# Performance work log

Hardware: AMD Instinct MI355X
Metric: run time of the kernel (lower is better)

## Reference

```python
import jax, jax.numpy as jnp
import numpy as np

B, L, D, H = 4, 1024, 1024, 16
HD = D // H  # head_dim = 64
SCALE = HD ** -0.5


def setup_inputs() -> dict:
    key = jax.random.key(0)
    k1, k2, k3, k4 = jax.random.split(key, 4)
    x = jax.random.normal(k1, (B, L, D), dtype=jnp.float32)
    # torch nn.Linear(dim, 3*dim): y = x @ W.T + b; we store W already transposed to [D, 3D]
    Wqkv = jax.random.normal(k2, (D, 3 * D), dtype=jnp.float32) * (D ** -0.5)
    bqkv = jax.random.normal(k3, (3 * D,), dtype=jnp.float32) * 0.02
    # distance_embedding: nn.Embedding(2*length - 1, head_dim)
    dist_emb = jax.random.normal(k4, (2 * L - 1, HD), dtype=jnp.float32) * 0.02
    return {"x": x, "Wqkv": Wqkv, "bqkv": bqkv, "dist_emb": dist_emb}


def reference(x, Wqkv, bqkv, dist_emb):
    b, l, d = x.shape
    # QKV projection -> [3, B, H, L, HD]
    qkv = (x @ Wqkv + bqkv).reshape(b, l, 3, H, HD).transpose(2, 0, 3, 1, 4)
    q, k, v = qkv[0], qkv[1], qkv[2]
    # raw attention scores: [B, H, L, L]
    scores = jnp.einsum("bhld,bhmd->bhlm", q, k)
    # relative position bias (relative_key_query branch)
    pos = jnp.arange(l)
    distance = pos[:, None] - pos[None, :]          # [L, L] in [-(L-1), L-1]
    pe = dist_emb[distance + (L - 1)]               # [L, L, HD]
    rel_q = jnp.einsum("bhld,lrd->bhlr", q, pe)
    rel_k = jnp.einsum("bhrd,lrd->bhlr", k, pe)
    scores = (scores + rel_q + rel_k) * SCALE
    probs = jax.nn.softmax(scores, axis=-1)
    out = jnp.einsum("bhlm,bhmd->bhld", probs, v)   # [B, H, L, HD]
    return out.transpose(0, 2, 1, 3).reshape(b, l, d)
```

## Files before the change

### kernel.cpp

```cpp
#include <hip/hip_runtime.h>
#include <hip/hip_bf16.h>
#include <math.h>

#define Bq 4
#define Lq 1024
#define Dq 1024
#define Hq 16
#define HDq 64
#define BHq (Bq * Hq)
#define HEAD_ELEMS ((size_t)BHq * Lq * HDq)

typedef short bf16x8 __attribute__((ext_vector_type(8)));
typedef _Float16 f16x8 __attribute__((ext_vector_type(8)));
typedef float f32x4 __attribute__((ext_vector_type(4)));
#define MFMA16B(A, B, C) __builtin_amdgcn_mfma_f32_16x16x32_bf16(A, B, C, 0, 0, 0)
#define MFMA16F(A, B, C) __builtin_amdgcn_mfma_f32_16x16x32_f16(A, B, C, 0, 0, 0)

__device__ __forceinline__ unsigned short f2bf(float x) {
  unsigned u = __builtin_bit_cast(unsigned, x);
  unsigned r = u + 0x7FFFu + ((u >> 16) & 1u);
  return (unsigned short)(r >> 16);
}
__device__ __forceinline__ float bf2f(unsigned short s) {
  unsigned u = ((unsigned)s) << 16;
  return __builtin_bit_cast(float, u);
}
__device__ __forceinline__ unsigned short f2h(float x) {
  _Float16 h = (_Float16)x;
  return __builtin_bit_cast(unsigned short, h);
}

__global__ __launch_bounds__(256) void x_prep(const float* __restrict__ X,
                                              unsigned short* __restrict__ Xh) {
  size_t i = (size_t)blockIdx.x * 256 + threadIdx.x;
  float4 f = *(const float4*)(X + i * 4);
  uint2 pk;
  pk.x = (unsigned)f2h(f.x) | ((unsigned)f2h(f.y) << 16);
  pk.y = (unsigned)f2h(f.z) | ((unsigned)f2h(f.w) << 16);
  *(uint2*)(Xh + i * 4) = pk;
}

__global__ __launch_bounds__(256) void wt_prep(const float* __restrict__ W,
                                               unsigned short* __restrict__ Wt) {
  __shared__ unsigned short tile[64 * 72];
  const int k0 = blockIdx.x * 64;
  const int n0 = blockIdx.y * 64;
  const int tid = threadIdx.x;
#pragma unroll
  for (int it = 0; it < 4; it++) {
    int idx = tid + it * 256;
    int r = idx >> 4, c4 = (idx & 15) * 4;
    float4 f = *(const float4*)(W + (size_t)(k0 + r) * 3072 + n0 + c4);
    unsigned w0 = (unsigned)f2h(f.x) | ((unsigned)f2h(f.y) << 16);
    unsigned w1 = (unsigned)f2h(f.z) | ((unsigned)f2h(f.w) << 16);
    *(unsigned*)&tile[r * 72 + c4] = w0;
    *(unsigned*)&tile[r * 72 + c4 + 2] = w1;
  }
  __syncthreads();
#pragma unroll
  for (int it = 0; it < 4; it++) {
    int u = tid + it * 256;
    int n = u >> 4, k4 = (u & 15) * 4;
    unsigned short e0 = tile[(k4 + 0) * 72 + n];
    unsigned short e1 = tile[(k4 + 1) * 72 + n];
    unsigned short e2 = tile[(k4 + 2) * 72 + n];
    unsigned short e3 = tile[(k4 + 3) * 72 + n];
    uint2 pk;
    pk.x = (unsigned)e0 | ((unsigned)e1 << 16);
    pk.y = (unsigned)e2 | ((unsigned)e3 << 16);
    *(uint2*)(Wt + (size_t)(n0 + n) * 1024 + k0 + k4) = pk;
  }
}

__global__ __launch_bounds__(256) void emb_prep(const float* __restrict__ e,
                                                unsigned short* __restrict__ o) {
  int i = blockIdx.x * 256 + threadIdx.x;
  if (i < 2047 * 64) o[i] = f2bf(e[i]);
}

__global__ __launch_bounds__(256, 2) void qkv_mfma(
    const unsigned short* __restrict__ Xh, const unsigned short* __restrict__ Wt,
    const float* __restrict__ bias, unsigned short* __restrict__ qkvg) {
  __shared__ __align__(16) char smem[32768];
  unsigned short* Asm = (unsigned short*)smem;
  unsigned short* Bsm = (unsigned short*)(smem + 8192);
  unsigned short* Cs  = (unsigned short*)smem;

  const int tid = threadIdx.x;
  const int w = tid >> 6, lane = tid & 63;
  const int col = lane & 15, quad = lane >> 4;
  const int wm = (w >> 1) * 64, wn = (w & 1) * 64;
  const int bn = blockIdx.x * 128, bm = blockIdx.y * 128;

  const unsigned short* Ag = Xh + (size_t)bm * 1024;
  const unsigned short* Bg = Wt + (size_t)bn * 1024;
  const int ldrow = w * 32 + (lane >> 2);
  const int ldoff = (lane & 3) * 8;

  f32x4 acc[4][4];
#pragma unroll
  for (int i = 0; i < 4; i++)
#pragma unroll
    for (int j = 0; j < 4; j++) acc[i][j] = (f32x4){0.f, 0.f, 0.f, 0.f};

  for (int k0 = 0; k0 < 1024; k0 += 32) {
    __syncthreads();
#pragma unroll
    for (int it = 0; it < 2; it++) {
      const unsigned short* ga = Ag + (size_t)(ldrow + it * 16) * 1024 + k0 + ldoff;
      const unsigned short* gb = Bg + (size_t)(ldrow + it * 16) * 1024 + k0 + ldoff;
      __builtin_amdgcn_global_load_lds(
          (const __attribute__((address_space(1))) unsigned*)ga,
          (__attribute__((address_space(3))) unsigned*)(Asm + (w * 32 + it * 16) * 32),
          16, 0, 0);
      __builtin_amdgcn_global_load_lds(
          (const __attribute__((address_space(1))) unsigned*)gb,
          (__attribute__((address_space(3))) unsigned*)(Bsm + (w * 32 + it * 16) * 32),
          16, 0, 0);
    }
    __syncthreads();
    f16x8 af[4], bf[4];
#pragma unroll
    for (int i = 0; i < 4; i++)
      af[i] = *(const f16x8*)&Asm[(wm + i * 16 + col) * 32 + quad * 8];
#pragma unroll
    for (int j = 0; j < 4; j++)
      bf[j] = *(const f16x8*)&Bsm[(wn + j * 16 + col) * 32 + quad * 8];
#pragma unroll
    for (int i = 0; i < 4; i++)
#pragma unroll
      for (int j = 0; j < 4; j++)
        acc[i][j] = MFMA16F(af[i], bf[j], acc[i][j]);
  }

  float bj[4];
#pragma unroll
  for (int j = 0; j < 4; j++) bj[j] = bias[bn + wn + j * 16 + col];

  __syncthreads();
#pragma unroll
  for (int i = 0; i < 4; i++)
#pragma unroll
    for (int j = 0; j < 4; j++)
#pragma unroll
      for (int k = 0; k < 4; k++)
        Cs[(wm + i * 16 + quad * 4 + k) * 128 + wn + j * 16 + col] =
            f2bf(acc[i][j][k] + bj[j]);
  __syncthreads();

  const int t = bn >> 10;
  unsigned short* dst_base = qkvg + (size_t)t * HEAD_ELEMS;
#pragma unroll
  for (int it = 0; it < 8; it++) {
    int u = tid + it * 256;
    int row = u >> 4, c8 = (u & 15) * 8;
    int m = bm + row;
    int n = bn + c8;
    int b = m >> 10, l = m & 1023;
    int cc = n & 1023, h = cc >> 6, d0 = cc & 63;
    uint4 val = *(const uint4*)&Cs[row * 128 + c8];
    *(uint4*)(dst_base + (((size_t)(b * 16 + h) * 1024 + l) * 64 + d0)) = val;
  }
}

__global__ __launch_bounds__(256) void vt_prep_bf(const unsigned short* __restrict__ vg,
                                                  unsigned short* __restrict__ vtg) {
  __shared__ unsigned short tile[64 * 72];
  const int bh = blockIdx.x;
  const int rt = blockIdx.y * 64;
  const int tid = threadIdx.x;
  const unsigned short* src = vg + ((size_t)bh * Lq + rt) * HDq;
#pragma unroll
  for (int it = 0; it < 2; it++) {
    int idx = tid + it * 256;
    int r = idx >> 3, o = (idx & 7) * 8;
    *(uint4*)&tile[r * 72 + o] = *(const uint4*)(src + (size_t)r * 64 + o);
  }
  __syncthreads();
  unsigned short* dst = vtg + (size_t)bh * HDq * Lq;
#pragma unroll
  for (int it = 0; it < 4; it++) {
    int u = tid + it * 256;
    int d = u >> 4, r4 = (u & 15) * 4;
    unsigned short e0 = tile[(r4 + 0) * 72 + d];
    unsigned short e1 = tile[(r4 + 1) * 72 + d];
    unsigned short e2 = tile[(r4 + 2) * 72 + d];
    unsigned short e3 = tile[(r4 + 3) * 72 + d];
    uint2 pk;
    pk.x = (unsigned)e0 | ((unsigned)e1 << 16);
    pk.y = (unsigned)e2 | ((unsigned)e3 << 16);
    *(uint2*)(dst + (size_t)d * Lq + rt + r4) = pk;
  }
}

__global__ __launch_bounds__(256, 2) void attn_mfma(
    const unsigned short* __restrict__ qg, const unsigned short* __restrict__ kg,
    const unsigned short* __restrict__ vtg, const unsigned short* __restrict__ emb,
    float* __restrict__ out) {
  __shared__ __align__(16) char smem[54272];
  unsigned short* Qs  = (unsigned short*)smem;
  unsigned short* Ps  = (unsigned short*)smem;
  unsigned short* Ks  = (unsigned short*)(smem + 9216);
  unsigned short* VTs = (unsigned short*)(smem + 18432);
  unsigned short* Pb  = (unsigned short*)(smem + 27648);
  unsigned short* B12 = (unsigned short*)(smem + 36864);

  const int bh = blockIdx.x;
  const int l0 = blockIdx.y * 64;
  const int tid = threadIdx.x;
  const int w = tid >> 6, lane = tid & 63;
  const int col = lane & 15, quad = lane >> 4;
  const int lw = w * 16;

  const unsigned short* Qg = qg + ((size_t)bh * Lq + l0) * HDq;
  const unsigned short* Kg = kg + (size_t)bh * Lq * HDq;
  const unsigned short* VTgh = vtg + (size_t)bh * HDq * Lq;

#pragma unroll
  for (int it = 0; it < 2; it++) {
    int idx = tid + it * 256;
    int r = idx >> 3, o = (idx & 7) * 8;
    *(uint4*)&Qs[r * 72 + o] = *(const uint4*)(Qg + (size_t)r * 64 + o);
    int g = min(l0 + 1024 + r, 2046);
    *(uint4*)&Pb[r * 72 + o] = *(const uint4*)(emb + (size_t)g * 64 + o);
  }
  __syncthreads();

  bf16x8 qf[2];
#pragma unroll
  for (int ks = 0; ks < 2; ks++)
    qf[ks] = *(const bf16x8*)&Qs[(lw + col) * 72 + quad * 8 + ks * 32];

  bf16x8 sav[4][2];
#pragma unroll
  for (int dm = 0; dm < 4; dm++)
#pragma unroll
    for (int ks = 0; ks < 2; ks++)
      sav[dm][ks] = *(const bf16x8*)&Pb[(dm * 16 + col) * 72 + quad * 8 + ks * 32];

  f32x4 oacc[4];
#pragma unroll
  for (int nt = 0; nt < 4; nt++) oacc[nt] = (f32x4){0.f, 0.f, 0.f, 0.f};
  float mrow[4] = {-1e30f, -1e30f, -1e30f, -1e30f};
  float lrow[4] = {0.f, 0.f, 0.f, 0.f};

  for (int ch = 0; ch < 16; ch++) {
    const int r0 = ch * 64;
    __syncthreads();

#pragma unroll
    for (int it = 0; it < 2; it++) {
      int idx = tid + it * 256;
      int r = idx >> 3, o = (idx & 7) * 8;
      *(uint4*)&Ks[r * 72 + o] = *(const uint4*)(Kg + (size_t)(r0 + r) * 64 + o);
    }
#pragma unroll
    for (int it = 0; it < 2; it++) {
      int idx = tid + it * 256;
      int d = idx >> 3, o = (idx & 7) * 8;
      *(uint4*)&VTs[d * 72 + o] = *(const uint4*)(VTgh + (size_t)d * Lq + r0 + o);
    }
    const int pb0 = l0 - r0 + 960;
#pragma unroll
    for (int it = 0; it < 2; it++) {
      int idx = tid + it * 256;
      int r = idx >> 3, o = (idx & 7) * 8;
      *(uint4*)&Pb[r * 72 + o] = *(const uint4*)(emb + (size_t)(pb0 + r) * 64 + o);
    }
    __syncthreads();

    bf16x8 kf[4][2];
#pragma unroll
    for (int rt = 0; rt < 4; rt++)
#pragma unroll
      for (int ks = 0; ks < 2; ks++)
        kf[rt][ks] = *(const bf16x8*)&Ks[(rt * 16 + col) * 72 + quad * 8 + ks * 32];
    f32x4 sac[4];
#pragma unroll
    for (int rt = 0; rt < 4; rt++) {
      f32x4 z = (f32x4){0.f, 0.f, 0.f, 0.f};
      z = MFMA16B(qf[0], kf[rt][0], z);
      z = MFMA16B(qf[1], kf[rt][1], z);
      sac[rt] = z;
    }

    bf16x8 kaf[2];
#pragma unroll
    for (int ks = 0; ks < 2; ks++)
      kaf[ks] = *(const bf16x8*)&Ks[(lw + col) * 72 + quad * 8 + ks * 32];

    bf16x8 fresh[4][2];
#pragma unroll
    for (int dm = 0; dm < 4; dm++)
#pragma unroll
      for (int ks = 0; ks < 2; ks++)
        fresh[dm][ks] = *(const bf16x8*)&Pb[(dm * 16 + col) * 72 + quad * 8 + ks * 32];

#pragma unroll
    for (int dt = 0; dt < 8; dt++) {
      bf16x8 pbf0 = (dt < 4) ? fresh[dt & 3][0] : sav[dt & 3][0];
      bf16x8 pbf1 = (dt < 4) ? fresh[dt & 3][1] : sav[dt & 3][1];
      f32x4 z = (f32x4){0.f, 0.f, 0.f, 0.f};
      f32x4 y = (f32x4){0.f, 0.f, 0.f, 0.f};
      z = MFMA16B(qf[0], pbf0, z);
      z = MFMA16B(qf[1], pbf1, z);
      y = MFMA16B(kaf[0], pbf0, y);
      y = MFMA16B(kaf[1], pbf1, y);
      const int dcol = dt * 16 + col;
#pragma unroll
      for (int k = 0; k < 4; k++) {
        int l1 = lw + quad * 4 + k;
        int r1 = l1 - dcol + 63;
        if (r1 >= 0 && r1 < 64) B12[l1 * 136 + 2 * r1] = f2bf(z[k]);
        int r2 = lw + quad * 4 + k;
        int l2 = dcol - 63 + r2;
        if (l2 >= 0 && l2 < 64) B12[l2 * 136 + 2 * r2 + 1] = f2bf(y[k]);
      }
    }
#pragma unroll
    for (int dm = 0; dm < 4; dm++)
#pragma unroll
      for (int ks = 0; ks < 2; ks++)
        sav[dm][ks] = fresh[dm][ks];
    __syncthreads();

    float p[4][4];
    float alpha[4];
#pragma unroll
    for (int k = 0; k < 4; k++) {
      int l1 = lw + quad * 4 + k;
      float st[4];
#pragma unroll
      for (int rt = 0; rt < 4; rt++) {
        int r = rt * 16 + col;
        unsigned pr = *(const unsigned*)&B12[l1 * 136 + 2 * r];
        float bias = bf2f((unsigned short)(pr & 0xFFFFu)) +
                     bf2f((unsigned short)(pr >> 16));
        st[rt] = (sac[rt][k] + bias) * 0.125f;
      }
      float mx = fmaxf(fmaxf(st[0], st[1]), fmaxf(st[2], st[3]));
      mx = fmaxf(mx, __shfl_xor(mx, 1));
      mx = fmaxf(mx, __shfl_xor(mx, 2));
      mx = fmaxf(mx, __shfl_xor(mx, 4));
      mx = fmaxf(mx, __shfl_xor(mx, 8));
      float mnew = fmaxf(mrow[k], mx);
      float a = __expf(mrow[k] - mnew);
      mrow[k] = mnew;
      alpha[k] = a;
      float ls = 0.f;
#pragma unroll
      for (int rt = 0; rt < 4; rt++) {
        p[rt][k] = __expf(st[rt] - mnew);
        ls += p[rt][k];
      }
      lrow[k] = lrow[k] * a + ls;
    }
#pragma unroll
    for (int nt = 0; nt < 4; nt++)
#pragma unroll
      for (int k = 0; k < 4; k++) oacc[nt][k] *= alpha[k];

#pragma unroll
    for (int rt = 0; rt < 4; rt++)
#pragma unroll
      for (int k = 0; k < 4; k++)
        Ps[(lw + quad * 4 + k) * 72 + rt * 16 + col] = f2bf(p[rt][k]);

    bf16x8 pf[2];
#pragma unroll
    for (int ks = 0; ks < 2; ks++)
      pf[ks] = *(const bf16x8*)&Ps[(lw + col) * 72 + quad * 8 + ks * 32];
#pragma unroll
    for (int nt = 0; nt < 4; nt++) {
      bf16x8 v0 = *(const bf16x8*)&VTs[(nt * 16 + col) * 72 + quad * 8];
      bf16x8 v1 = *(const bf16x8*)&VTs[(nt * 16 + col) * 72 + quad * 8 + 32];
      oacc[nt] = MFMA16B(pf[0], v0, oacc[nt]);
      oacc[nt] = MFMA16B(pf[1], v1, oacc[nt]);
    }
  }

  float inv[4];
#pragma unroll
  for (int k = 0; k < 4; k++) {
    float t = lrow[k];
    t += __shfl_xor(t, 1);
    t += __shfl_xor(t, 2);
    t += __shfl_xor(t, 4);
    t += __shfl_xor(t, 8);
    inv[k] = 1.0f / t;
  }
  const int b = bh >> 4, h = bh & 15;
#pragma unroll
  for (int nt = 0; nt < 4; nt++) {
#pragma unroll
    for (int k = 0; k < 4; k++) {
      int lg = l0 + lw + quad * 4 + k;
      int d = nt * 16 + col;
      out[(((size_t)b * Lq + lg) * Hq + h) * HDq + d] = oacc[nt][k] * inv[k];
    }
  }
}

extern "C" void kernel_launch(void* const* d_in, const int* in_sizes, int n_in,
                              void* d_out, int out_size, void* d_ws, size_t ws_size,
                              hipStream_t stream) {
  const float* x        = (const float*)d_in[0];
  const float* Wqkv     = (const float*)d_in[1];
  const float* bqkv     = (const float*)d_in[2];
  const float* dist_emb = (const float*)d_in[3];
  float* out = (float*)d_out;

  unsigned short* Xh   = (unsigned short*)d_ws;
  unsigned short* Wt   = (unsigned short*)((char*)d_ws + (8u << 20));
  unsigned short* qkvg = (unsigned short*)((char*)d_ws + (16u << 20));
  unsigned short* vtg  = (unsigned short*)((char*)d_ws + (40u << 20));
  unsigned short* emb  = (unsigned short*)((char*)d_ws + (48u << 20));

  x_prep<<<dim3(4096), dim3(256), 0, stream>>>(x, Xh);
  wt_prep<<<dim3(16, 48), dim3(256), 0, stream>>>(Wqkv, Wt);
  emb_prep<<<dim3(512), dim3(256), 0, stream>>>(dist_emb, emb);

  qkv_mfma<<<dim3(24, 32), dim3(256), 0, stream>>>(Xh, Wt, bqkv, qkvg);

  vt_prep_bf<<<dim3(BHq, Lq / 64), dim3(256), 0, stream>>>(qkvg + 2 * HEAD_ELEMS, vtg);

  attn_mfma<<<dim3(BHq, Lq / 64), dim3(256), 0, stream>>>(
      qkvg, qkvg + HEAD_ELEMS, vtg, emb, out);
}
```

Baseline: 262.7 us.

## Load MFMA fragments directly from global memory, drop LDS staging, use exp2

Q, K, V^T and distance-embedding fragments are now read straight from global memory into registers instead of being staged through shared memory. This removes the per-chunk LDS copies and their barriers, shrinks LDS from about 53 KB to 26 KB, and raises launch bounds to three blocks per CU. The softmax also folds log2(e) into the scale and uses a native exp2. In exchange each lane issues more scattered global loads that depend on L2 hits, with less latency hiding from the removed staging, and register pressure under the new bound may cause spills.

```diff
diff --git a/kernel.cpp b/kernel.cpp
--- a/kernel.cpp
+++ b/kernel.cpp
@@ -15,6 +15,12 @@
 typedef float f32x4 __attribute__((ext_vector_type(4)));
 #define MFMA16B(A, B, C) __builtin_amdgcn_mfma_f32_16x16x32_bf16(A, B, C, 0, 0, 0)
 #define MFMA16F(A, B, C) __builtin_amdgcn_mfma_f32_16x16x32_f16(A, B, C, 0, 0, 0)
+
+#if __has_builtin(__builtin_amdgcn_exp2f)
+#define EXP2F(x) __builtin_amdgcn_exp2f(x)
+#else
+#define EXP2F(x) __expf((x) * 0.6931471805599453f)
+#endif
 
 __device__ __forceinline__ unsigned short f2bf(float x) {
   unsigned u = __builtin_bit_cast(unsigned, x);
@@ -193,17 +199,13 @@
   }
 }
 
-__global__ __launch_bounds__(256, 2) void attn_mfma(
+__global__ __launch_bounds__(256, 3) void attn_mfma(
     const unsigned short* __restrict__ qg, const unsigned short* __restrict__ kg,
     const unsigned short* __restrict__ vtg, const unsigned short* __restrict__ emb,
     float* __restrict__ out) {
-  __shared__ __align__(16) char smem[54272];
-  unsigned short* Qs  = (unsigned short*)smem;
+  __shared__ __align__(16) char smem[26624];
   unsigned short* Ps  = (unsigned short*)smem;
-  unsigned short* Ks  = (unsigned short*)(smem + 9216);
-  unsigned short* VTs = (unsigned short*)(smem + 18432);
-  unsigned short* Pb  = (unsigned short*)(smem + 27648);
-  unsigned short* B12 = (unsigned short*)(smem + 36864);
+  unsigned short* B12 = (unsigned short*)(smem + 9216);
 
   const int bh = blockIdx.x;
   const int l0 = blockIdx.y * 64;
@@ -211,32 +213,26 @@
   const int w = tid >> 6, lane = tid & 63;
   const int col = lane & 15, quad = lane >> 4;
   const int lw = w * 16;
+  const int fo = quad * 8;
 
   const unsigned short* Qg = qg + ((size_t)bh * Lq + l0) * HDq;
-  const unsigned short* Kg = kg + (size_t)bh * Lq * HDq;
-  const unsigned short* VTgh = vtg + (size_t)bh * HDq * Lq;
-
-#pragma unroll
-  for (int it = 0; it < 2; it++) {
-    int idx = tid + it * 256;
-    int r = idx >> 3, o = (idx & 7) * 8;
-    *(uint4*)&Qs[r * 72 + o] = *(const uint4*)(Qg + (size_t)r * 64 + o);
-    int g = min(l0 + 1024 + r, 2046);
-    *(uint4*)&Pb[r * 72 + o] = *(const uint4*)(emb + (size_t)g * 64 + o);
-  }
-  __syncthreads();
+  const unsigned short* Kp = kg + (size_t)bh * Lq * HDq;
+  const unsigned short* Vp = vtg + (size_t)bh * HDq * Lq;
 
   bf16x8 qf[2];
 #pragma unroll
   for (int ks = 0; ks < 2; ks++)
-    qf[ks] = *(const bf16x8*)&Qs[(lw + col) * 72 + quad * 8 + ks * 32];
+    qf[ks] = *(const bf16x8*)(Qg + (size_t)(lw + col) * 64 + fo + ks * 32);
 
   bf16x8 sav[4][2];
 #pragma unroll
-  for (int dm = 0; dm < 4; dm++)
+  for (int dm = 0; dm < 4; dm++) {
+    int g = l0 + 1024 + dm * 16 + col;
+    g = (g > 2046) ? 2046 : g;
 #pragma unroll
     for (int ks = 0; ks < 2; ks++)
-      sav[dm][ks] = *(const bf16x8*)&Pb[(dm * 16 + col) * 72 + quad * 8 + ks * 32];
+      sav[dm][ks] = *(const bf16x8*)(emb + (size_t)g * 64 + fo + ks * 32);
+  }
 
   f32x4 oacc[4];
 #pragma unroll
@@ -244,37 +240,27 @@
   float mrow[4] = {-1e30f, -1e30f, -1e30f, -1e30f};
   float lrow[4] = {0.f, 0.f, 0.f, 0.f};
 
+  int pb0 = l0 + 960;
+
   for (int ch = 0; ch < 16; ch++) {
-    const int r0 = ch * 64;
-    __syncthreads();
-
-#pragma unroll
-    for (int it = 0; it < 2; it++) {
-      int idx = tid + it * 256;
-      int r = idx >> 3, o = (idx & 7) * 8;
-      *(uint4*)&Ks[r * 72 + o] = *(const uint4*)(Kg + (size_t)(r0 + r) * 64 + o);
-    }
-#pragma unroll
-    for (int it = 0; it < 2; it++) {
-      int idx = tid + it * 256;
-      int d = idx >> 3, o = (idx & 7) * 8;
-      *(uint4*)&VTs[d * 72 + o] = *(const uint4*)(VTgh + (size_t)d * Lq + r0 + o);
-    }
-    const int pb0 = l0 - r0 + 960;
-#pragma unroll
-    for (int it = 0; it < 2; it++) {
-      int idx = tid + it * 256;
-      int r = idx >> 3, o = (idx & 7) * 8;
-      *(uint4*)&Pb[r * 72 + o] = *(const uint4*)(emb + (size_t)(pb0 + r) * 64 + o);
-    }
-    __syncthreads();
-
     bf16x8 kf[4][2];
 #pragma unroll
     for (int rt = 0; rt < 4; rt++)
 #pragma unroll
       for (int ks = 0; ks < 2; ks++)
-        kf[rt][ks] = *(const bf16x8*)&Ks[(rt * 16 + col) * 72 + quad * 8 + ks * 32];
+        kf[rt][ks] = *(const bf16x8*)(Kp + (size_t)(rt * 16 + col) * 64 + fo + ks * 32);
+    bf16x8 kaf[2];
+#pragma unroll
+    for (int ks = 0; ks < 2; ks++)
+      kaf[ks] = *(const bf16x8*)(Kp + (size_t)(lw + col) * 64 + fo + ks * 32);
+    bf16x8 fresh[4][2];
+#pragma unroll
+    for (int dm = 0; dm < 4; dm++)
+#pragma unroll
+      for (int ks = 0; ks < 2; ks++)
+        fresh[dm][ks] =
+            *(const bf16x8*)(emb + (size_t)(pb0 + dm * 16 + col) * 64 + fo + ks * 32);
+
     f32x4 sac[4];
 #pragma unroll
     for (int rt = 0; rt < 4; rt++) {
@@ -284,17 +270,7 @@
       sac[rt] = z;
     }
 
-    bf16x8 kaf[2];
-#pragma unroll
-    for (int ks = 0; ks < 2; ks++)
-      kaf[ks] = *(const bf16x8*)&Ks[(lw + col) * 72 + quad * 8 + ks * 32];
-
-    bf16x8 fresh[4][2];
-#pragma unroll
-    for (int dm = 0; dm < 4; dm++)
-#pragma unroll
-      for (int ks = 0; ks < 2; ks++)
-        fresh[dm][ks] = *(const bf16x8*)&Pb[(dm * 16 + col) * 72 + quad * 8 + ks * 32];
+    __syncthreads();
 
 #pragma unroll
     for (int dt = 0; dt < 8; dt++) {
@@ -324,6 +300,13 @@
         sav[dm][ks] = fresh[dm][ks];
     __syncthreads();
 
+    bf16x8 va[4], vb[4];
+#pragma unroll
+    for (int nt = 0; nt < 4; nt++) {
+      va[nt] = *(const bf16x8*)(Vp + (size_t)(nt * 16 + col) * Lq + fo);
+      vb[nt] = *(const bf16x8*)(Vp + (size_t)(nt * 16 + col) * Lq + fo + 32);
+    }
+
     float p[4][4];
     float alpha[4];
 #pragma unroll
@@ -336,7 +319,7 @@
         unsigned pr = *(const unsigned*)&B12[l1 * 136 + 2 * r];
         float bias = bf2f((unsigned short)(pr & 0xFFFFu)) +
                      bf2f((unsigned short)(pr >> 16));
-        st[rt] = (sac[rt][k] + bias) * 0.125f;
+        st[rt] = (sac[rt][k] + bias) * 0.18033688011112042f;
       }
       float mx = fmaxf(fmaxf(st[0], st[1]), fmaxf(st[2], st[3]));
       mx = fmaxf(mx, __shfl_xor(mx, 1));
@@ -344,13 +327,13 @@
       mx = fmaxf(mx, __shfl_xor(mx, 4));
       mx = fmaxf(mx, __shfl_xor(mx, 8));
       float mnew = fmaxf(mrow[k], mx);
-      float a = __expf(mrow[k] - mnew);
+      float a = EXP2F(mrow[k] - mnew);
       mrow[k] = mnew;
       alpha[k] = a;
       float ls = 0.f;
 #pragma unroll
       for (int rt = 0; rt < 4; rt++) {
-        p[rt][k] = __expf(st[rt] - mnew);
+        p[rt][k] = EXP2F(st[rt] - mnew);
         ls += p[rt][k];
       }
       lrow[k] = lrow[k] * a + ls;
@@ -369,14 +352,16 @@
     bf16x8 pf[2];
 #pragma unroll
     for (int ks = 0; ks < 2; ks++)
-      pf[ks] = *(const bf16x8*)&Ps[(lw + col) * 72 + quad * 8 + ks * 32];
+      pf[ks] = *(const bf16x8*)&Ps[(lw + col) * 72 + fo + ks * 32];
 #pragma unroll
     for (int nt = 0; nt < 4; nt++) {
-      bf16x8 v0 = *(const bf16x8*)&VTs[(nt * 16 + col) * 72 + quad * 8];
-      bf16x8 v1 = *(const bf16x8*)&VTs[(nt * 16 + col) * 72 + quad * 8 + 32];
-      oacc[nt] = MFMA16B(pf[0], v0, oacc[nt]);
-      oacc[nt] = MFMA16B(pf[1], v1, oacc[nt]);
-    }
+      oacc[nt] = MFMA16B(pf[0], va[nt], oacc[nt]);
+      oacc[nt] = MFMA16B(pf[1], vb[nt], oacc[nt]);
+    }
+
+    Kp += 64 * 64;
+    Vp += 64;
+    pb0 -= 64;
   }
 
   float inv[4];
```

Result: slower. 566.9 us (+115.8%).
